# Kernel optimization log

Measured on AMD Instinct MI355X. Metric: run time of the kernel, lower is better.

## Reference

```python
import jax, jax.numpy as jnp
import numpy as np

H, W, HEADS, DIM_HEAD, SLICE = 256, 256, 8, 64, 64
SCALE = DIM_HEAD ** -0.5


def _conv(x_nhwc, w_hwio, b):
    y = jax.lax.conv_general_dilated(
        x_nhwc, w_hwio, window_strides=(1, 1), padding='SAME',
        dimension_numbers=('NHWC', 'HWIO', 'NHWC'))
    return y + b


def setup_inputs() -> dict:
    key = jax.random.key(0)
    ks = jax.random.split(key, 13)
    B, N, C, inner = 2, H * W, 128, HEADS * DIM_HEAD
    s = lambda k, shp, sc: jax.random.normal(k, shp, jnp.float32) * sc
    return {
        'x': s(ks[0], (B, N, C), 1.0),
        'Wfx': s(ks[1], (3, 3, C, inner), 0.05),
        'bfx': s(ks[2], (inner,), 0.02),
        'Wx': s(ks[3], (3, 3, C, inner), 0.05),
        'bx': s(ks[4], (inner,), 0.02),
        'Wslice': s(ks[5], (SLICE, DIM_HEAD), 0.1),
        'bslice': s(ks[6], (SLICE,), 0.02),
        'temperature': jnp.ones((1, HEADS, 1, 1), jnp.float32) * 0.5,
        'Wq': s(ks[7], (DIM_HEAD, DIM_HEAD), 0.1),
        'Wk': s(ks[8], (DIM_HEAD, DIM_HEAD), 0.1),
        'Wv': s(ks[9], (DIM_HEAD, DIM_HEAD), 0.1),
        'Wout': s(ks[10], (C, inner), 0.05),
        'bout': s(ks[11], (C,), 0.02),
    }


def reference(x, Wfx, bfx, Wx, bx, Wslice, bslice, temperature, Wq, Wk, Wv, Wout, bout):
    B, N, C = x.shape
    xg = x.reshape(B, H, W, C)                       # NHWC grid
    # conv QKV-style projections -> [B, heads, N, dim_head]
    def to_heads(y):
        return y.reshape(B, N, HEADS, DIM_HEAD).transpose(0, 2, 1, 3)
    fx_mid = to_heads(_conv(xg, Wfx, bfx))           # [B,h,N,d]
    x_mid = to_heads(_conv(xg, Wx, bx))              # [B,h,N,d]
    # slice assignment weights: softmax over slices with clamped temperature
    temp = jnp.clip(temperature, 0.1, 5.0)           # [1,h,1,1]
    logits = (jnp.einsum('bhnd,gd->bhng', x_mid, Wslice) + bslice) / temp
    slice_weights = jax.nn.softmax(logits, axis=-1)  # [B,h,N,G]
    slice_norm = slice_weights.sum(axis=2)           # [B,h,G]
    slice_token = jnp.einsum('bhnc,bhng->bhgc', fx_mid, slice_weights)
    slice_token = slice_token / (slice_norm + 1e-5)[..., None]  # [B,h,G,d]
    # small attention over slice tokens
    q = jnp.einsum('bhgd,ed->bhge', slice_token, Wq)
    k = jnp.einsum('bhgd,ed->bhge', slice_token, Wk)
    v = jnp.einsum('bhgd,ed->bhge', slice_token, Wv)
    attn = jax.nn.softmax(jnp.einsum('bhge,bhfe->bhgf', q, k) * SCALE, axis=-1)
    out_slice = jnp.einsum('bhgf,bhfe->bhge', attn, v)           # [B,h,G,d]
    # scatter back to tokens
    out_x = jnp.einsum('bhgc,bhng->bhnc', out_slice, slice_weights)
    out_x = out_x.transpose(0, 2, 1, 3).reshape(B, N, HEADS * DIM_HEAD)
    return jnp.einsum('bni,oi->bno', out_x, Wout) + bout
```

## Files before the change

### kernel.cpp

```cpp
#include <hip/hip_runtime.h>


typedef _Float16 f16;
typedef _Float16 f16x8 __attribute__((ext_vector_type(8)));
typedef _Float16 f16x4 __attribute__((ext_vector_type(4)));
typedef float    f32x4 __attribute__((ext_vector_type(4)));

static const size_t OFF_PADX = 0;
static const size_t OFF_WCAT = 17040384;
static const size_t OFF_ST   = 19399680;
static const size_t OFF_NORM = 19530752;
static const size_t OFF_OS   = 19532800;
static const size_t OFF_PT   = 19663872;
static const size_t OFF_XMID = 19794944;
static const size_t OFF_FXT  = 86903808;

__device__ __forceinline__ void ldsdma16(f16* lds, const f16* g) {
  __builtin_amdgcn_global_load_lds((__attribute__((address_space(1))) void*)g,
                                   (__attribute__((address_space(3))) void*)lds,
                                   16, 0, 0);
}

__global__ __launch_bounds__(256) void pad_kernel(const float* __restrict__ xb,
                                                  f16* __restrict__ padx) {
  int idx = blockIdx.x * 256 + threadIdx.x;
  if (idx >= 258 * 258 * 16) return;
  int c8 = (idx & 15) * 8;
  int r  = idx >> 4;
  int jp = r % 258;
  int ip = r / 258;
  f16x8 v;
  if (ip == 0 || ip == 257 || jp == 0 || jp == 257) {
#pragma unroll
    for (int j = 0; j < 8; ++j) v[j] = (f16)0.0f;
  } else {
    const float* src = xb + ((size_t)(ip - 1) * 256 + (jp - 1)) * 128 + c8;
#pragma unroll
    for (int j = 0; j < 8; ++j) v[j] = (f16)src[j];
  }
  *(f16x8*)(padx + (size_t)r * 128 + c8) = v;
}

__global__ __launch_bounds__(256) void prepw_kernel(const float* __restrict__ Wfx,
                                                    const float* __restrict__ Wx,
                                                    f16* __restrict__ wcat) {
  int idx = blockIdx.x * 256 + threadIdx.x;
  if (idx >= 9 * 1024 * 128) return;
  int ci = idx & 127;
  int t  = idx >> 7;
  int co = t & 1023;
  int tap = t >> 10;
  float v = (co < 512) ? Wfx[(size_t)(tap * 128 + ci) * 512 + co]
                       : Wx[(size_t)(tap * 128 + ci) * 512 + (co - 512)];
  wcat[idx] = (f16)v;
}

__global__ __launch_bounds__(256, 2) void conv_kernel(const f16* __restrict__ padx,
                                                      const f16* __restrict__ wcat,
                                                      const float* __restrict__ bfx,
                                                      const float* __restrict__ bx,
                                                      f16* __restrict__ xmid,
                                                      f16* __restrict__ fxT) {
  __shared__ f16 As[130 * 64];
  __shared__ f16 Bs[3 * 128 * 64];
  int tid = threadIdx.x;
  int nt = blockIdx.x & 7;
  int mt = blockIdx.x >> 3;
  int i  = mt >> 1;
  int j0 = (mt & 1) * 128;
  int n0 = nt * 128;
  int lane = tid & 63, wave = tid >> 6;
  int ln15 = lane & 15, quad = lane >> 4;
  int wm = wave & 1, wn = wave >> 1;

  f32x4 acc[4][4] = {};

  for (int di = 0; di < 3; ++di) {
    const f16* aRow = padx + ((size_t)(i + di) * 258 + j0) * 128;
    for (int kc = 0; kc < 128; kc += 64) {
#pragma unroll
      for (int ph = 0; ph < 5; ++ph) {
        int s = ph * 256 + tid;
        if (s < 1040) {
          int rr = s >> 3;
          int qq = ((s & 7) ^ (rr & 7)) * 8;
          ldsdma16(&As[(ph * 256 + wave * 64) * 8], aRow + (size_t)rr * 128 + kc + qq);
        }
      }
#pragma unroll
      for (int ph = 0; ph < 12; ++ph) {
        int s2 = ph * 256 + tid;
        int dj = s2 >> 10;
        int sB = s2 & 1023;
        int rr = sB >> 3;
        int qq = ((sB & 7) ^ (rr & 7)) * 8;
        ldsdma16(&Bs[(ph * 256 + wave * 64) * 8],
                 wcat + ((size_t)((di * 3 + dj) * 1024 + n0 + rr)) * 128 + kc + qq);
      }
      __syncthreads();
#pragma unroll
      for (int dj = 0; dj < 3; ++dj) {
#pragma unroll
        for (int ks = 0; ks < 2; ++ks) {
          int q = ks * 4 + quad;
          f16x8 af[4], bfr[4];
#pragma unroll
          for (int xx = 0; xx < 4; ++xx) {
            int t  = dj + wm * 64 + xx * 16 + ln15;
            int rb = wn * 64 + xx * 16 + ln15;
            af[xx]  = *(const f16x8*)(&As[t * 64 + ((q ^ (t & 7)) * 8)]);
            bfr[xx] = *(const f16x8*)(&Bs[dj * 8192 + rb * 64 + ((q ^ (rb & 7)) * 8)]);
          }
#pragma unroll
          for (int mf = 0; mf < 4; ++mf)
#pragma unroll
            for (int nf = 0; nf < 4; ++nf)
              acc[mf][nf] = __builtin_amdgcn_mfma_f32_16x16x32_f16(af[mf], bfr[nf],
                                                                   acc[mf][nf], 0, 0, 0);
        }
      }
      __syncthreads();
    }
  }

  size_t token0 = (size_t)i * 256 + j0;
  if (nt < 4) {
    f16* tile = Bs;
#pragma unroll
    for (int nf = 0; nf < 4; ++nf) {
      int colLoc = wn * 64 + nf * 16 + ln15;
      float bias = bfx[n0 + colLoc];
#pragma unroll
      for (int mf = 0; mf < 4; ++mf) {
        int tokBase = wm * 64 + mf * 16 + quad * 4;
        f16x4 pk;
#pragma unroll
        for (int v = 0; v < 4; ++v) pk[v] = (f16)(acc[mf][nf][v] + bias);
        *(f16x4*)(&tile[colLoc * 136 + tokBase]) = pk;
      }
    }
    __syncthreads();
#pragma unroll
    for (int it2 = 0; it2 < 8; ++it2) {
      int s = it2 * 256 + tid;
      int c = s >> 4, t8 = s & 15;
      f16x8 vv = *(const f16x8*)(&tile[c * 136 + t8 * 8]);
      *(f16x8*)(fxT + (size_t)(n0 + c) * 65536 + token0 + t8 * 8) = vv;
    }
  } else {
#pragma unroll
    for (int nf = 0; nf < 4; ++nf) {
      int col = n0 + wn * 64 + nf * 16 + ln15;
      float bias = bx[col - 512];
#pragma unroll
      for (int mf = 0; mf < 4; ++mf) {
        int rbase = wm * 64 + mf * 16 + quad * 4;
#pragma unroll
        for (int v = 0; v < 4; ++v)
          xmid[(size_t)(token0 + rbase + v) * 512 + (col - 512)] =
              (f16)(acc[mf][nf][v] + bias);
      }
    }
  }
}

#define WS_S 72
#define WT_S 264
__global__ __launch_bounds__(256, 2) void slice_kernel(f16* __restrict__ xmid,
                                                       const f16* __restrict__ fxT,
                                                       const float* __restrict__ Wslice,
                                                       const float* __restrict__ bslice,
                                                       const float* __restrict__ temperature,
                                                       float* __restrict__ ST,
                                                       float* __restrict__ snorm) {
  __shared__ f16 Ws[64 * WS_S];
  __shared__ f16 Wt[64 * WT_S];
  __shared__ float red[64 * 65];
  __shared__ float redn[64];
  int tid = threadIdx.x;
  int h = blockIdx.x >> 6;
  int chunk = blockIdx.x & 63;
  int tok0 = chunk * 1024;
  int lane = tid & 63, wave = tid >> 6;
  int ln15 = lane & 15, quad = lane >> 4;

  for (int s = tid; s < 4096; s += 256)
    Ws[(s >> 6) * WS_S + (s & 63)] = (f16)Wslice[s];
  if (tid < 64) redn[tid] = 0.f;
  float tc = temperature[h];
  tc = fminf(fmaxf(tc, 0.1f), 5.0f);
  float invt = 1.0f / tc;
  float bsv[4];
#pragma unroll
  for (int nf = 0; nf < 4; ++nf) bsv[nf] = bslice[nf * 16 + ln15];
  __syncthreads();

  f32x4 acc2[4][4] = {};
  float naccv[4] = {};

  for (int it = 0; it < 4; ++it) {
    int tsub = it * 256 + wave * 64;
    f32x4 accA[4][4] = {};
#pragma unroll
    for (int kq = 0; kq < 2; ++kq) {
      f16x8 bf[4];
#pragma unroll
      for (int nf = 0; nf < 4; ++nf)
        bf[nf] = *(const f16x8*)(&Ws[(nf * 16 + ln15) * WS_S + kq * 32 + quad * 8]);
#pragma unroll
      for (int mf = 0; mf < 4; ++mf) {
        f16x8 af = *(const f16x8*)(xmid + (size_t)(tok0 + tsub + mf * 16 + ln15) * 512 +
                                   h * 64 + kq * 32 + quad * 8);
#pragma unroll
        for (int nf = 0; nf < 4; ++nf)
          accA[mf][nf] = __builtin_amdgcn_mfma_f32_16x16x32_f16(af, bf[nf], accA[mf][nf],
                                                                0, 0, 0);
      }
    }
#pragma unroll
    for (int mf = 0; mf < 4; ++mf) {
#pragma unroll
      for (int v = 0; v < 4; ++v) {
        float l[4];
#pragma unroll
        for (int nf = 0; nf < 4; ++nf) l[nf] = (accA[mf][nf][v] + bsv[nf]) * invt;
        float lm = fmaxf(fmaxf(l[0], l[1]), fmaxf(l[2], l[3]));
#pragma unroll
        for (int off = 1; off < 16; off <<= 1) lm = fmaxf(lm, __shfl_xor(lm, off, 64));
        float e[4], ssum = 0.f;
#pragma unroll
        for (int nf = 0; nf < 4; ++nf) { e[nf] = __expf(l[nf] - lm); ssum += e[nf]; }
#pragma unroll
        for (int off = 1; off < 16; off <<= 1) ssum += __shfl_xor(ssum, off, 64);
        float winv = 1.0f / ssum;
        int t_loc = tsub + mf * 16 + quad * 4 + v;
        int t_str = wave * 64 + mf * 16 + quad * 4 + v;
        f16* wrow = xmid + (size_t)(tok0 + t_loc) * 512 + h * 64;
#pragma unroll
        for (int nf = 0; nf < 4; ++nf) {
          float w = e[nf] * winv;
          naccv[nf] += w;
          f16 wh = (f16)w;
          wrow[nf * 16 + ln15] = wh;
          Wt[(nf * 16 + ln15) * WT_S + t_str] = wh;
        }
      }
    }
#pragma unroll
    for (int kq = 0; kq < 2; ++kq) {
      int kof = wave * 64 + kq * 32 + quad * 8;
      f16x8 bfB[4];
#pragma unroll
      for (int nf = 0; nf < 4; ++nf)
        bfB[nf] = *(const f16x8*)(fxT + (size_t)(h * 64 + nf * 16 + ln15) * 65536 +
                                  tok0 + it * 256 + kof);
#pragma unroll
      for (int mf = 0; mf < 4; ++mf) {
        f16x8 afB = *(const f16x8*)(&Wt[(mf * 16 + ln15) * WT_S + kof]);
#pragma unroll
        for (int nf = 0; nf < 4; ++nf)
          acc2[mf][nf] = __builtin_amdgcn_mfma_f32_16x16x32_f16(afB, bfB[nf],
                                                                acc2[mf][nf], 0, 0, 0);
      }
    }
  }

#pragma unroll
  for (int nf = 0; nf < 4; ++nf) atomicAdd(&redn[nf * 16 + ln15], naccv[nf]);

  for (int s = 0; s < 4; ++s) {
    if (wave == s) {
#pragma unroll
      for (int mf = 0; mf < 4; ++mf)
#pragma unroll
        for (int nf = 0; nf < 4; ++nf)
#pragma unroll
          for (int v = 0; v < 4; ++v) {
            int g = mf * 16 + quad * 4 + v;
            int d = nf * 16 + ln15;
            if (s == 0) red[g * 65 + d] = acc2[mf][nf][v];
            else        red[g * 65 + d] += acc2[mf][nf][v];
          }
    }
    __syncthreads();
  }
  float* stp = ST + (size_t)h * 4096;
  for (int s2 = tid; s2 < 4096; s2 += 256)
    atomicAdd(&stp[s2], red[(s2 >> 6) * 65 + (s2 & 63)]);
  if (tid < 64) atomicAdd(&snorm[h * 64 + tid], redn[tid]);
}

__global__ __launch_bounds__(256) void attn_kernel(const float* __restrict__ ST,
                                                   const float* __restrict__ snorm,
                                                   const float* __restrict__ Wq,
                                                   const float* __restrict__ Wk,
                                                   const float* __restrict__ Wv,
                                                   float* __restrict__ OS) {
  int h = blockIdx.x;
  __shared__ float tok[64 * 65];
  __shared__ float qs[64 * 65];
  __shared__ float ksm[64 * 65];
  __shared__ f16 vsm[64 * 65];
  int tid = threadIdx.x;
  const float* stp = ST + (size_t)h * 4096;
  const float* snp = snorm + (size_t)h * 64;
  for (int s = tid; s < 4096; s += 256) {
    int g = s >> 6, d = s & 63;
    tok[g * 65 + d] = stp[s] / (snp[g] + 1e-5f);
  }
  __syncthreads();
  int g = tid >> 2, p16 = (tid & 3) * 16;
  for (int e0 = 0; e0 < 16; ++e0) {
    int e = p16 + e0;
    const float* wq = Wq + e * 64;
    const float* wk = Wk + e * 64;
    const float* wv = Wv + e * 64;
    float aq = 0, ak = 0, av = 0;
#pragma unroll 8
    for (int d = 0; d < 64; ++d) {
      float tv = tok[g * 65 + d];
      aq += tv * wq[d];
      ak += tv * wk[d];
      av += tv * wv[d];
    }
    qs[g * 65 + e] = aq;
    ksm[g * 65 + e] = ak;
    vsm[g * 65 + e] = (f16)av;
  }
  __syncthreads();
  float* sc = tok;
  for (int f0 = 0; f0 < 16; ++f0) {
    int f = p16 + f0;
    float s = 0;
#pragma unroll 8
    for (int e = 0; e < 64; ++e) s += qs[g * 65 + e] * ksm[f * 65 + e];
    sc[g * 65 + f] = s * 0.125f;
  }
  __syncthreads();
  if (tid < 64) {
    float m = -1e30f;
    for (int f = 0; f < 64; ++f) m = fmaxf(m, sc[tid * 65 + f]);
    float ssum = 0;
    for (int f = 0; f < 64; ++f) {
      float e = __expf(sc[tid * 65 + f] - m);
      sc[tid * 65 + f] = e;
      ssum += e;
    }
    float inv = 1.0f / ssum;
    for (int f = 0; f < 64; ++f) sc[tid * 65 + f] *= inv;
  }
  __syncthreads();
  for (int e0 = 0; e0 < 16; ++e0) {
    int e = p16 + e0;
    float o = 0;
#pragma unroll 8
    for (int f = 0; f < 64; ++f) o += sc[g * 65 + f] * (float)vsm[f * 65 + e];
    OS[(size_t)h * 4096 + g * 64 + e] = o;
  }
}

__global__ __launch_bounds__(256) void pt_kernel(const float* __restrict__ OS,
                                                 const float* __restrict__ Wout,
                                                 f16* __restrict__ PT) {
  int h = blockIdx.x;
  __shared__ float os[64 * 65];
  int tid = threadIdx.x;
  for (int s = tid; s < 4096; s += 256) os[(s >> 6) * 65 + (s & 63)] = OS[(size_t)h * 4096 + s];
  __syncthreads();
  int o = tid >> 1, gh = (tid & 1) * 32;
  const float* wr = Wout + (size_t)o * 512 + h * 64;
  float wreg[64];
#pragma unroll
  for (int d = 0; d < 64; ++d) wreg[d] = wr[d];
  for (int gg = 0; gg < 32; ++gg) {
    int g = gh + gg;
    float s = 0;
#pragma unroll
    for (int d = 0; d < 64; ++d) s += os[g * 65 + d] * wreg[d];
    PT[(size_t)o * 512 + h * 64 + g] = (f16)s;
  }
}

__global__ __launch_bounds__(256, 2) void final_kernel(const f16* __restrict__ xmid,
                                                       const f16* __restrict__ PT,
                                                       const float* __restrict__ bout,
                                                       float* __restrict__ outb) {
  __shared__ f16 As[128 * 64];
  __shared__ f16 Bs[128 * 64];
  int tid = threadIdx.x;
  int tok0 = blockIdx.x << 7;
  int lane = tid & 63, wave = tid >> 6;
  int ln15 = lane & 15, quad = lane >> 4;
  int wm = wave & 1, wn = wave >> 1;
  int rr[4], qq8[4];
#pragma unroll
  for (int ph = 0; ph < 4; ++ph) {
    int s = ph * 256 + tid;
    rr[ph] = s >> 3;
    qq8[ph] = ((s & 7) ^ (rr[ph] & 7)) * 8;
  }
  int wbase = wave * 512;
  f32x4 acc[4][4] = {};
  const f16* aB = xmid + (size_t)tok0 * 512;
  const f16* bB = PT;
  for (int kc = 0; kc < 512; kc += 64) {
#pragma unroll
    for (int ph = 0; ph < 4; ++ph) {
      ldsdma16(&As[ph * 2048 + wbase], aB + (size_t)rr[ph] * 512 + kc + qq8[ph]);
      ldsdma16(&Bs[ph * 2048 + wbase], bB + (size_t)rr[ph] * 512 + kc + qq8[ph]);
    }
    __syncthreads();
#pragma unroll
    for (int ks = 0; ks < 2; ++ks) {
      f16x8 af[4], bfr[4];
      int q = ks * 4 + quad;
#pragma unroll
      for (int xx = 0; xx < 4; ++xx) {
        int ra = wm * 64 + xx * 16 + ln15;
        int rb = wn * 64 + xx * 16 + ln15;
        af[xx]  = *(const f16x8*)(&As[ra * 64 + (q ^ (ra & 7)) * 8]);
        bfr[xx] = *(const f16x8*)(&Bs[rb * 64 + (q ^ (rb & 7)) * 8]);
      }
#pragma unroll
      for (int mf = 0; mf < 4; ++mf)
#pragma unroll
        for (int nf = 0; nf < 4; ++nf)
          acc[mf][nf] = __builtin_amdgcn_mfma_f32_16x16x32_f16(af[mf], bfr[nf],
                                                               acc[mf][nf], 0, 0, 0);
    }
    __syncthreads();
  }
#pragma unroll
  for (int nf = 0; nf < 4; ++nf) {
    int col = wn * 64 + nf * 16 + ln15;
    float bo = bout[col];
#pragma unroll
    for (int mf = 0; mf < 4; ++mf) {
      int rbase = wm * 64 + mf * 16 + quad * 4;
#pragma unroll
      for (int v = 0; v < 4; ++v)
        outb[(size_t)(tok0 + rbase + v) * 128 + col] = acc[mf][nf][v] + bo;
    }
  }
}

extern "C" void kernel_launch(void* const* d_in, const int* in_sizes, int n_in,
                              void* d_out, int out_size, void* d_ws, size_t ws_size,
                              hipStream_t stream) {
  const float* x    = (const float*)d_in[0];
  const float* Wfx  = (const float*)d_in[1];
  const float* bfx  = (const float*)d_in[2];
  const float* Wx   = (const float*)d_in[3];
  const float* bx   = (const float*)d_in[4];
  const float* Wsl  = (const float*)d_in[5];
  const float* bsl  = (const float*)d_in[6];
  const float* temp = (const float*)d_in[7];
  const float* Wq   = (const float*)d_in[8];
  const float* Wk   = (const float*)d_in[9];
  const float* Wv   = (const float*)d_in[10];
  const float* Wout = (const float*)d_in[11];
  const float* bout = (const float*)d_in[12];
  float* out = (float*)d_out;
  char* ws = (char*)d_ws;

  f16*  padx = (f16*)(ws + OFF_PADX);
  f16*  wcat = (f16*)(ws + OFF_WCAT);
  float* ST  = (float*)(ws + OFF_ST);
  float* nrm = (float*)(ws + OFF_NORM);
  float* OS  = (float*)(ws + OFF_OS);
  f16*  PT   = (f16*)(ws + OFF_PT);
  f16*  xmid = (f16*)(ws + OFF_XMID);
  f16*  fxT  = (f16*)(ws + OFF_FXT);

  prepw_kernel<<<4608, 256, 0, stream>>>(Wfx, Wx, wcat);
  for (int b = 0; b < 2; ++b) {
    const float* xb = x + (size_t)b * 65536 * 128;
    float* outb = out + (size_t)b * 65536 * 128;
    hipMemsetAsync(ws + OFF_ST, 0, 131072 + 2048, stream);
    pad_kernel<<<4161, 256, 0, stream>>>(xb, padx);
    conv_kernel<<<4096, 256, 0, stream>>>(padx, wcat, bfx, bx, xmid, fxT);
    slice_kernel<<<512, 256, 0, stream>>>(xmid, fxT, Wsl, bsl, temp, ST, nrm);
    attn_kernel<<<8, 256, 0, stream>>>(ST, nrm, Wq, Wk, Wv, OS);
    pt_kernel<<<8, 256, 0, stream>>>(OS, Wout, PT);
    final_kernel<<<512, 256, 0, stream>>>(xmid, PT, bout, outb);
  }
}
```

Baseline: 841.9 us.

## Restructure conv GEMM with full-row tiles, double-buffered weight taps and 512 threads

The conv kernel now processes a full 256-token image row per block with 512 threads and stages the whole 128-channel K dimension at once. Weight taps are double-buffered so the next tap's LDS DMA overlaps the current tap's MFMA work, and the dj=2 A fragments are held in registers so the next row's A tile can load early. The aim is to hide global-to-LDS latency and halve redundant A reloads. In exchange it uses about 128KB of shared memory and more registers, which may limit occupancy.

```diff
diff --git a/kernel.cpp b/kernel.cpp
--- a/kernel.cpp
+++ b/kernel.cpp
@@ -55,77 +55,130 @@
   wcat[idx] = (f16)v;
 }
 
-__global__ __launch_bounds__(256, 2) void conv_kernel(const f16* __restrict__ padx,
+__global__ __launch_bounds__(512, 2) void conv_kernel(const f16* __restrict__ padx,
                                                       const f16* __restrict__ wcat,
                                                       const float* __restrict__ bfx,
                                                       const float* __restrict__ bx,
                                                       f16* __restrict__ xmid,
                                                       f16* __restrict__ fxT) {
-  __shared__ f16 As[130 * 64];
-  __shared__ f16 Bs[3 * 128 * 64];
+  __shared__ f16 smem[65792];
+  f16* As  = smem;
+  f16* Bs0 = smem + 33024;
+  f16* Bs1 = smem + 49408;
   int tid = threadIdx.x;
   int nt = blockIdx.x & 7;
   int mt = blockIdx.x >> 3;
-  int i  = mt >> 1;
-  int j0 = (mt & 1) * 128;
   int n0 = nt * 128;
   int lane = tid & 63, wave = tid >> 6;
   int ln15 = lane & 15, quad = lane >> 4;
-  int wm = wave & 1, wn = wave >> 1;
+  int wm = wave & 3, wn = wave >> 2;
 
   f32x4 acc[4][4] = {};
 
+  auto stageA = [&](int di) {
+    const f16* aRow = padx + (size_t)(mt + di) * (258 * 128);
+#pragma unroll
+    for (int ph = 0; ph < 9; ++ph) {
+      int s = ph * 512 + tid;
+      if (ph < 8 || s < 4128) {
+        int rr = s >> 4;
+        int qq = ((s & 15) ^ (rr & 7)) * 8;
+        ldsdma16(&As[(ph * 512 + wave * 64) * 8], aRow + (size_t)rr * 128 + qq);
+      }
+    }
+  };
+  auto stageB = [&](int tap, f16* dst) {
+    const f16* bRow = wcat + (size_t)(tap * 1024 + n0) * 128;
+#pragma unroll
+    for (int ph = 0; ph < 4; ++ph) {
+      int s = ph * 512 + tid;
+      int rr = s >> 4;
+      int qq = ((s & 15) ^ (rr & 7)) * 8;
+      ldsdma16(&dst[(ph * 512 + wave * 64) * 8], bRow + (size_t)rr * 128 + qq);
+    }
+  };
+  auto computeTap = [&](int dj, const f16* B) {
+#pragma unroll
+    for (int ks = 0; ks < 4; ++ks) {
+      int q = ks * 4 + quad;
+      f16x8 af[4], bf[4];
+#pragma unroll
+      for (int xx = 0; xx < 4; ++xx) {
+        int t  = dj + wm * 64 + xx * 16 + ln15;
+        int rb = wn * 64 + xx * 16 + ln15;
+        af[xx] = *(const f16x8*)(&As[t * 128 + ((q ^ (t & 7)) * 8)]);
+        bf[xx] = *(const f16x8*)(&B[rb * 128 + ((q ^ (rb & 7)) * 8)]);
+      }
+      __builtin_amdgcn_s_setprio(1);
+#pragma unroll
+      for (int mf = 0; mf < 4; ++mf)
+#pragma unroll
+        for (int nf = 0; nf < 4; ++nf)
+          acc[mf][nf] = __builtin_amdgcn_mfma_f32_16x16x32_f16(af[mf], bf[nf],
+                                                               acc[mf][nf], 0, 0, 0);
+      __builtin_amdgcn_s_setprio(0);
+    }
+  };
+
+  stageA(0);
+  stageB(0, Bs0);
+  __syncthreads();
+
+  int cur = 0;
+#pragma unroll 1
   for (int di = 0; di < 3; ++di) {
-    const f16* aRow = padx + ((size_t)(i + di) * 258 + j0) * 128;
-    for (int kc = 0; kc < 128; kc += 64) {
-#pragma unroll
-      for (int ph = 0; ph < 5; ++ph) {
-        int s = ph * 256 + tid;
-        if (s < 1040) {
-          int rr = s >> 3;
-          int qq = ((s & 7) ^ (rr & 7)) * 8;
-          ldsdma16(&As[(ph * 256 + wave * 64) * 8], aRow + (size_t)rr * 128 + kc + qq);
+    stageB(di * 3 + 1, cur ? Bs0 : Bs1);
+    computeTap(0, cur ? Bs1 : Bs0);
+    __syncthreads();
+    cur ^= 1;
+    stageB(di * 3 + 2, cur ? Bs0 : Bs1);
+    computeTap(1, cur ? Bs1 : Bs0);
+    __syncthreads();
+    cur ^= 1;
+    if (di < 2) {
+      f16x8 afr[4][4];
+#pragma unroll
+      for (int ks = 0; ks < 4; ++ks) {
+        int q = ks * 4 + quad;
+#pragma unroll
+        for (int mf = 0; mf < 4; ++mf) {
+          int t = 2 + wm * 64 + mf * 16 + ln15;
+          afr[ks][mf] = *(const f16x8*)(&As[t * 128 + ((q ^ (t & 7)) * 8)]);
         }
       }
-#pragma unroll
-      for (int ph = 0; ph < 12; ++ph) {
-        int s2 = ph * 256 + tid;
-        int dj = s2 >> 10;
-        int sB = s2 & 1023;
-        int rr = sB >> 3;
-        int qq = ((sB & 7) ^ (rr & 7)) * 8;
-        ldsdma16(&Bs[(ph * 256 + wave * 64) * 8],
-                 wcat + ((size_t)((di * 3 + dj) * 1024 + n0 + rr)) * 128 + kc + qq);
-      }
       __syncthreads();
-#pragma unroll
-      for (int dj = 0; dj < 3; ++dj) {
-#pragma unroll
-        for (int ks = 0; ks < 2; ++ks) {
-          int q = ks * 4 + quad;
-          f16x8 af[4], bfr[4];
-#pragma unroll
-          for (int xx = 0; xx < 4; ++xx) {
-            int t  = dj + wm * 64 + xx * 16 + ln15;
-            int rb = wn * 64 + xx * 16 + ln15;
-            af[xx]  = *(const f16x8*)(&As[t * 64 + ((q ^ (t & 7)) * 8)]);
-            bfr[xx] = *(const f16x8*)(&Bs[dj * 8192 + rb * 64 + ((q ^ (rb & 7)) * 8)]);
-          }
-#pragma unroll
-          for (int mf = 0; mf < 4; ++mf)
-#pragma unroll
-            for (int nf = 0; nf < 4; ++nf)
-              acc[mf][nf] = __builtin_amdgcn_mfma_f32_16x16x32_f16(af[mf], bfr[nf],
-                                                                   acc[mf][nf], 0, 0, 0);
+      stageA(di + 1);
+      stageB(di * 3 + 3, cur ? Bs0 : Bs1);
+      const f16* B = cur ? Bs1 : Bs0;
+#pragma unroll
+      for (int ks = 0; ks < 4; ++ks) {
+        int q = ks * 4 + quad;
+        f16x8 bf[4];
+#pragma unroll
+        for (int xx = 0; xx < 4; ++xx) {
+          int rb = wn * 64 + xx * 16 + ln15;
+          bf[xx] = *(const f16x8*)(&B[rb * 128 + ((q ^ (rb & 7)) * 8)]);
         }
+        __builtin_amdgcn_s_setprio(1);
+#pragma unroll
+        for (int mf = 0; mf < 4; ++mf)
+#pragma unroll
+          for (int nf = 0; nf < 4; ++nf)
+            acc[mf][nf] = __builtin_amdgcn_mfma_f32_16x16x32_f16(afr[ks][mf], bf[nf],
+                                                                 acc[mf][nf], 0, 0, 0);
+        __builtin_amdgcn_s_setprio(0);
       }
       __syncthreads();
-    }
-  }
-
-  size_t token0 = (size_t)i * 256 + j0;
+      cur ^= 1;
+    } else {
+      computeTap(2, cur ? Bs1 : Bs0);
+    }
+  }
+
+  size_t token0 = (size_t)mt * 256;
   if (nt < 4) {
-    f16* tile = Bs;
+    __syncthreads();
+    f16* tile = smem;
 #pragma unroll
     for (int nf = 0; nf < 4; ++nf) {
       int colLoc = wn * 64 + nf * 16 + ln15;
@@ -136,15 +189,15 @@
         f16x4 pk;
 #pragma unroll
         for (int v = 0; v < 4; ++v) pk[v] = (f16)(acc[mf][nf][v] + bias);
-        *(f16x4*)(&tile[colLoc * 136 + tokBase]) = pk;
+        *(f16x4*)(&tile[colLoc * 264 + tokBase]) = pk;
       }
     }
     __syncthreads();
 #pragma unroll
     for (int it2 = 0; it2 < 8; ++it2) {
-      int s = it2 * 256 + tid;
-      int c = s >> 4, t8 = s & 15;
-      f16x8 vv = *(const f16x8*)(&tile[c * 136 + t8 * 8]);
+      int s = it2 * 512 + tid;
+      int c = s >> 5, t8 = s & 31;
+      f16x8 vv = *(const f16x8*)(&tile[c * 264 + t8 * 8]);
       *(f16x8*)(fxT + (size_t)(n0 + c) * 65536 + token0 + t8 * 8) = vv;
     }
   } else {
@@ -476,9 +529,9 @@
   for (int b = 0; b < 2; ++b) {
     const float* xb = x + (size_t)b * 65536 * 128;
     float* outb = out + (size_t)b * 65536 * 128;
-    hipMemsetAsync(ws + OFF_ST, 0, 131072 + 2048, stream);
+    (void)hipMemsetAsync(ws + OFF_ST, 0, 131072 + 2048, stream);
     pad_kernel<<<4161, 256, 0, stream>>>(xb, padx);
-    conv_kernel<<<4096, 256, 0, stream>>>(padx, wcat, bfx, bx, xmid, fxT);
+    conv_kernel<<<2048, 512, 0, stream>>>(padx, wcat, bfx, bx, xmid, fxT);
     slice_kernel<<<512, 256, 0, stream>>>(xmid, fxT, Wsl, bsl, temp, ST, nrm);
     attn_kernel<<<8, 256, 0, stream>>>(ST, nrm, Wq, Wk, Wv, OS);
     pt_kernel<<<8, 256, 0, stream>>>(OS, Wout, PT);
```

After: 868.7 us. 1.03x slower.

## Double-buffer conv implicit-GEMM LDS staging per tap to overlap loads with MFMA

Applied to the files above, without the earlier changes.

Restructures the conv kernel main loop into 18 phases (3 row taps × 2 K chunks × 3 column taps). Each phase stages one tap's B tile and, every third phase, a new A row tile into alternate LDS buffers while MFMAs run on the current buffers. The per-phase B footprint shrinks from three taps to one, so LDS stays about the same size despite double buffering. It also raises wave priority around the MFMA bursts. The trade is more barriers (one per phase instead of one per K chunk) and a finer-grained DMA issue pattern.

```diff
diff --git a/kernel.cpp b/kernel.cpp
--- a/kernel.cpp
+++ b/kernel.cpp
@@ -61,8 +61,11 @@
                                                       const float* __restrict__ bx,
                                                       f16* __restrict__ xmid,
                                                       f16* __restrict__ fxT) {
-  __shared__ f16 As[130 * 64];
-  __shared__ f16 Bs[3 * 128 * 64];
+  __shared__ f16 smem[33024];
+  f16* As0 = smem;
+  f16* As1 = smem + 8320;
+  f16* Bs0 = smem + 16640;
+  f16* Bs1 = smem + 24832;
   int tid = threadIdx.x;
   int nt = blockIdx.x & 7;
   int mt = blockIdx.x >> 3;
@@ -75,57 +78,73 @@
 
   f32x4 acc[4][4] = {};
 
-  for (int di = 0; di < 3; ++di) {
-    const f16* aRow = padx + ((size_t)(i + di) * 258 + j0) * 128;
-    for (int kc = 0; kc < 128; kc += 64) {
-#pragma unroll
-      for (int ph = 0; ph < 5; ++ph) {
-        int s = ph * 256 + tid;
-        if (s < 1040) {
-          int rr = s >> 3;
-          int qq = ((s & 7) ^ (rr & 7)) * 8;
-          ldsdma16(&As[(ph * 256 + wave * 64) * 8], aRow + (size_t)rr * 128 + kc + qq);
-        }
-      }
-#pragma unroll
-      for (int ph = 0; ph < 12; ++ph) {
-        int s2 = ph * 256 + tid;
-        int dj = s2 >> 10;
-        int sB = s2 & 1023;
-        int rr = sB >> 3;
-        int qq = ((sB & 7) ^ (rr & 7)) * 8;
-        ldsdma16(&Bs[(ph * 256 + wave * 64) * 8],
-                 wcat + ((size_t)((di * 3 + dj) * 1024 + n0 + rr)) * 128 + kc + qq);
-      }
-      __syncthreads();
-#pragma unroll
-      for (int dj = 0; dj < 3; ++dj) {
-#pragma unroll
-        for (int ks = 0; ks < 2; ++ks) {
-          int q = ks * 4 + quad;
-          f16x8 af[4], bfr[4];
-#pragma unroll
-          for (int xx = 0; xx < 4; ++xx) {
-            int t  = dj + wm * 64 + xx * 16 + ln15;
-            int rb = wn * 64 + xx * 16 + ln15;
-            af[xx]  = *(const f16x8*)(&As[t * 64 + ((q ^ (t & 7)) * 8)]);
-            bfr[xx] = *(const f16x8*)(&Bs[dj * 8192 + rb * 64 + ((q ^ (rb & 7)) * 8)]);
-          }
-#pragma unroll
-          for (int mf = 0; mf < 4; ++mf)
-#pragma unroll
-            for (int nf = 0; nf < 4; ++nf)
-              acc[mf][nf] = __builtin_amdgcn_mfma_f32_16x16x32_f16(af[mf], bfr[nf],
-                                                                   acc[mf][nf], 0, 0, 0);
-        }
-      }
-      __syncthreads();
-    }
+  auto stageA = [&](int di, int kc, f16* dst) {
+#pragma unroll
+    for (int ph = 0; ph < 5; ++ph) {
+      int s = ph * 256 + tid;
+      if (ph < 4 || s < 1040) {
+        int rr = s >> 3;
+        int qq = ((s & 7) ^ (rr & 7)) * 8;
+        ldsdma16(&dst[(ph * 256 + wave * 64) * 8],
+                 padx + ((size_t)(i + di) * 258 + j0 + rr) * 128 + kc + qq);
+      }
+    }
+  };
+  auto stageB = [&](int tap, int kc, f16* dst) {
+#pragma unroll
+    for (int ph = 0; ph < 4; ++ph) {
+      int s = ph * 256 + tid;
+      int rr = s >> 3;
+      int qq = ((s & 7) ^ (rr & 7)) * 8;
+      ldsdma16(&dst[(ph * 256 + wave * 64) * 8],
+               wcat + ((size_t)(tap * 1024 + n0 + rr)) * 128 + kc + qq);
+    }
+  };
+  auto computePhase = [&](int dj, const f16* A, const f16* B) {
+#pragma unroll
+    for (int ks = 0; ks < 2; ++ks) {
+      int q = ks * 4 + quad;
+      f16x8 af[4], bfr[4];
+#pragma unroll
+      for (int xx = 0; xx < 4; ++xx) {
+        int t  = dj + wm * 64 + xx * 16 + ln15;
+        int rb = wn * 64 + xx * 16 + ln15;
+        af[xx]  = *(const f16x8*)(&A[t * 64 + ((q ^ (t & 7)) * 8)]);
+        bfr[xx] = *(const f16x8*)(&B[rb * 64 + ((q ^ (rb & 7)) * 8)]);
+      }
+      __builtin_amdgcn_s_setprio(1);
+#pragma unroll
+      for (int mf = 0; mf < 4; ++mf)
+#pragma unroll
+        for (int nf = 0; nf < 4; ++nf)
+          acc[mf][nf] = __builtin_amdgcn_mfma_f32_16x16x32_f16(af[mf], bfr[nf],
+                                                               acc[mf][nf], 0, 0, 0);
+      __builtin_amdgcn_s_setprio(0);
+    }
+  };
+
+  stageA(0, 0, As0);
+  stageB(0, 0, Bs0);
+  __syncthreads();
+
+#pragma unroll
+  for (int p = 0; p < 18; ++p) {
+    int dj   = p % 3;
+    int dikc = p / 3;
+    if (p + 1 < 18) {
+      int np = p + 1;
+      int ndj = np % 3, ndikc = np / 3;
+      int ndi = ndikc >> 1, nkc = (ndikc & 1) * 64;
+      stageB(ndi * 3 + ndj, nkc, (np & 1) ? Bs1 : Bs0);
+      if (ndj == 0) stageA(ndi, nkc, (ndikc & 1) ? As1 : As0);
+    }
+    computePhase(dj, (dikc & 1) ? As1 : As0, (p & 1) ? Bs1 : Bs0);
+    __syncthreads();
   }
 
   size_t token0 = (size_t)i * 256 + j0;
   if (nt < 4) {
-    f16* tile = Bs;
+    f16* tile = smem;
 #pragma unroll
     for (int nf = 0; nf < 4; ++nf) {
       int colLoc = wn * 64 + nf * 16 + ln15;
@@ -476,7 +495,7 @@
   for (int b = 0; b < 2; ++b) {
     const float* xb = x + (size_t)b * 65536 * 128;
     float* outb = out + (size_t)b * 65536 * 128;
-    hipMemsetAsync(ws + OFF_ST, 0, 131072 + 2048, stream);
+    (void)hipMemsetAsync(ws + OFF_ST, 0, 131072 + 2048, stream);
     pad_kernel<<<4161, 256, 0, stream>>>(xb, padx);
     conv_kernel<<<4096, 256, 0, stream>>>(padx, wcat, bfx, bx, xmid, fxT);
     slice_kernel<<<512, 256, 0, stream>>>(xmid, fxT, Wsl, bsl, temp, ST, nrm);
```

New measurement: 830.0 us. No clear change (-1.4%).
